# Optimization experiments

Measured on AMD Instinct MI355X. Metric: run time of the kernel, lower is better.

## Reference

```python
import jax, jax.numpy as jnp
from jax import lax
import numpy as np

B, T = 32, 64
E = 64        # embed_dim
U = 32        # num_measurements
D0, D1 = 300, 100
S = 9         # speaker_num
CELL = 64     # output_cell_dim
C = 6         # n_classes
EPS = 1e-12


def setup_inputs() -> dict:
    key = jax.random.key(0)
    ks = jax.random.split(key, 16)
    sc = 1.0 / np.sqrt(E)
    n = lambda i, shape, s=1.0: (jax.random.normal(ks[i], shape, jnp.float32) * s)
    return {
        "x0": n(0, (B, T, D0)),
        "x1": n(1, (B, T, D1)),
        "smask": jax.random.uniform(ks[2], (B, T, S), jnp.float32),
        "umask": jnp.ones((B, T), jnp.float32),
        "W_ih0": n(3, (4 * E, D0), sc), "W_hh0": n(4, (4 * E, E), sc),
        "b_ih0": n(5, (4 * E,), sc), "b_hh0": n(6, (4 * E,), sc),
        "W_ih1": n(7, (4 * E, D1), sc), "W_hh1": n(8, (4 * E, E), sc),
        "b_ih1": n(9, (4 * E,), sc), "b_hh1": n(10, (4 * E,), sc),
        "phase_table": jax.random.uniform(ks[11], (S, E), jnp.float32, -np.pi, np.pi),
        "meas_kernel": jax.random.uniform(ks[12], (U, E, 2), jnp.float32),
        "W1": n(13, (CELL, 2 * U), 0.1), "b1": jnp.zeros((CELL,), jnp.float32),
        "W2": n(14, (C, CELL), 0.1), "b2": jnp.zeros((C,), jnp.float32),
    }


def _lstm_tanh(x, um, Wih, Whh, bih, bhh):
    # torch.nn.LSTMCell (gate order i,f,g,o) + extra tanh applied to h each step;
    # the tanh-ed h is carried as the recurrent state (dropout = identity in eval).
    b, t, _ = x.shape
    e = Whh.shape[1]

    def step(carry, inp):
        h, c = carry
        xt, ut = inp
        g = (xt * ut[:, None]) @ Wih.T + bih + h @ Whh.T + bhh
        i, f, gg, o = jnp.split(g, 4, axis=-1)
        c = jax.nn.sigmoid(f) * c + jax.nn.sigmoid(i) * jnp.tanh(gg)
        h = jnp.tanh(jax.nn.sigmoid(o) * jnp.tanh(c))
        return (h, c), h

    h0 = jnp.zeros((b, e), x.dtype)
    _, hs = lax.scan(step, (h0, h0), (jnp.swapaxes(x, 0, 1), um.T))
    return jnp.swapaxes(hs, 0, 1)  # (B,T,E)


def _measure(amp, phase, kernel):
    # pure state v = cos(phase)*amp + i sin(phase)*amp; rho = |v><v|
    r = jnp.cos(phase) * amp
    im = jnp.sin(phase) * amp
    rho_r = jnp.einsum('bti,btj->btij', r, r) + jnp.einsum('bti,btj->btij', im, im)
    rho_i = jnp.einsum('bti,btj->btij', im, r) - jnp.einsum('bti,btj->btij', r, im)
    u = kernel.shape[0]
    norm = jnp.clip(jnp.linalg.norm(kernel.reshape(u, -1), axis=-1), EPS)
    kn = kernel / norm[:, None, None]
    kr, ki = kn[..., 0], kn[..., 1]
    Pr = jnp.einsum('ui,uj->uij', kr, kr) + jnp.einsum('ui,uj->uij', ki, ki)
    Pi = jnp.einsum('ui,uj->uij', ki, kr) - jnp.einsum('ui,uj->uij', kr, ki)
    return jnp.einsum('btij,uij->btu', rho_r, Pr) - jnp.einsum('btij,uij->btu', rho_i, Pi)


def reference(x0, x1, smask, umask, W_ih0, W_hh0, b_ih0, b_hh0,
              W_ih1, W_hh1, b_ih1, b_hh1, phase_table, meas_kernel,
              W1, b1, W2, b2):
    h0 = _lstm_tanh(x0, umask, W_ih0, W_hh0, b_ih0, b_hh0)
    h1 = _lstm_tanh(x1, umask, W_ih1, W_hh1, b_ih1, b_hh1)
    norm = lambda h: h / jnp.clip(jnp.linalg.norm(h, axis=-1, keepdims=True), EPS)
    phase = phase_table[jnp.argmax(smask, axis=-1)]  # (B,T,E); table shared by both modalities
    m = jnp.concatenate([_measure(norm(h0), phase, meas_kernel),
                         _measure(norm(h1), phase, meas_kernel)], axis=-1)
    hid = jax.nn.relu(m @ W1.T + b1)
    pred = jnp.tanh(hid @ W2.T + b2)
    return jax.nn.log_softmax(pred, axis=2)
```

## Files before the change

### kernel.cpp

```cpp
#include <hip/hip_runtime.h>

typedef unsigned short ushort_t;
typedef unsigned int uint_t;

__device__ __forceinline__ float bf2f(ushort_t v) {
  union { uint_t u; float f; } x; x.u = ((uint_t)v) << 16; return x.f;
}
__device__ __forceinline__ float lo16(uint_t u) {
  union { uint_t u; float f; } x; x.u = u << 16; return x.f;
}
__device__ __forceinline__ float hi16(uint_t u) {
  union { uint_t u; float f; } x; x.u = u & 0xffff0000u; return x.f;
}
__device__ __forceinline__ ushort_t f2bf(float f) {
  union { float f; uint_t u; } x; x.f = f;
  uint_t u = x.u;
  uint_t r = (u + 0x7fffu + ((u >> 16) & 1u)) >> 16;
  return (ushort_t)r;
}
__device__ __forceinline__ bool is_bf16(const void* um) {
  return *(const uint_t*)um == 0x3F803F80u;
}
__device__ __forceinline__ float ld_dual(const void* p, int i, bool isb) {
  return isb ? bf2f(((const ushort_t*)p)[i]) : ((const float*)p)[i];
}
__device__ __forceinline__ float fsig(float x) { return 1.f / (1.f + __expf(-x)); }
__device__ __forceinline__ float ftanh(float x) { return 2.f / (1.f + __expf(-2.f * x)) - 1.f; }

template <int D, bool ISB>
__device__ __forceinline__ void proj_body(
    const void* __restrict__ x, const void* __restrict__ um,
    const void* __restrict__ Wih, const void* __restrict__ bih,
    const void* __restrict__ bhh, float* __restrict__ xw, float* xs)
{
  const int tid = threadIdx.x;
  const int r0 = blockIdx.x * 8;
  for (int i = tid; i < 8 * D; i += 256) {
    const int r = i / D;
    xs[i] = ld_dual(x, r0 * D + i, ISB) * ld_dual(um, r0 + r, ISB);
  }
  __syncthreads();
  float acc[8];
#pragma unroll
  for (int r = 0; r < 8; ++r) acc[r] = 0.f;
#pragma unroll 5
  for (int k = 0; k < D; k += 4) {
    float w0, w1, w2, w3;
    if (ISB) {
      const ushort_t* wr = (const ushort_t*)Wih + tid * D;
      const uint2 wu = *(const uint2*)(wr + k);
      w0 = lo16(wu.x); w1 = hi16(wu.x); w2 = lo16(wu.y); w3 = hi16(wu.y);
    } else {
      const float* wr = (const float*)Wih + tid * D;
      const float4 wv = *(const float4*)(wr + k);
      w0 = wv.x; w1 = wv.y; w2 = wv.z; w3 = wv.w;
    }
#pragma unroll
    for (int r = 0; r < 8; ++r) {
      const float4 xv = *(const float4*)(xs + r * D + k);
      acc[r] = fmaf(xv.x, w0, acc[r]);
      acc[r] = fmaf(xv.y, w1, acc[r]);
      acc[r] = fmaf(xv.z, w2, acc[r]);
      acc[r] = fmaf(xv.w, w3, acc[r]);
    }
  }
  const float bias = ld_dual(bih, tid, ISB) + ld_dual(bhh, tid, ISB);
#pragma unroll
  for (int r = 0; r < 8; ++r)
    xw[(r0 + r) * 256 + tid] = acc[r] + bias;
}

__global__ __launch_bounds__(256) void proj_both(
    const void* __restrict__ x0, const void* __restrict__ x1,
    const void* __restrict__ um,
    const void* __restrict__ Wih0, const void* __restrict__ bih0,
    const void* __restrict__ bhh0,
    const void* __restrict__ Wih1, const void* __restrict__ bih1,
    const void* __restrict__ bhh1,
    float* __restrict__ xw0, float* __restrict__ xw1)
{
  __shared__ __align__(16) float xs[8 * 300];
  const bool isb = is_bf16(um);
  if (blockIdx.y == 0) {
    if (isb) proj_body<300, true>(x0, um, Wih0, bih0, bhh0, xw0, xs);
    else     proj_body<300, false>(x0, um, Wih0, bih0, bhh0, xw0, xs);
  } else {
    if (isb) proj_body<100, true>(x1, um, Wih1, bih1, bhh1, xw1, xs);
    else     proj_body<100, false>(x1, um, Wih1, bih1, bhh1, xw1, xs);
  }
}

__global__ __launch_bounds__(256) void lstm_k(
    const float* __restrict__ xw0, const float* __restrict__ xw1,
    const void* __restrict__ Whh0, const void* __restrict__ Whh1,
    const void* __restrict__ um,
    float* __restrict__ h0r, float* __restrict__ h1r)
{
  const int bid = blockIdx.x;
  const int l = bid >> 5;
  const int b = bid & 31;
  const float* xw = (l ? xw1 : xw0) + b * 64 * 256;
  const void* Whh = (l ? Whh1 : Whh0);
  float* hr = (l ? h1r : h0r) + b * 64 * 64;
  const int tid = threadIdx.x;
  const int e = tid & 63;
  const bool isb = is_bf16(um);

  float w[64];
  if (isb) {
    const ushort_t* wr = (const ushort_t*)Whh + tid * 64;
#pragma unroll
    for (int j = 0; j < 64; j += 8) {
      const uint4 v = *(const uint4*)(wr + j);
      w[j + 0] = lo16(v.x); w[j + 1] = hi16(v.x);
      w[j + 2] = lo16(v.y); w[j + 3] = hi16(v.y);
      w[j + 4] = lo16(v.z); w[j + 5] = hi16(v.z);
      w[j + 6] = lo16(v.w); w[j + 7] = hi16(v.w);
    }
  } else {
    const float* wr = (const float*)Whh + tid * 64;
#pragma unroll
    for (int j = 0; j < 64; j += 4) {
      const float4 v = *(const float4*)(wr + j);
      w[j + 0] = v.x; w[j + 1] = v.y; w[j + 2] = v.z; w[j + 3] = v.w;
    }
  }
  __shared__ __align__(16) float hsh[64];
  __shared__ float gsh[2][256];
  float c = 0.f;
  if (tid < 64) hsh[tid] = 0.f;
  __syncthreads();
  float gin = xw[tid];
  for (int s = 0; s < 64; ++s) {
    float gnext = 0.f;
    if (s < 63) gnext = xw[(s + 1) * 256 + tid];
    float a0 = gin, a1 = 0.f, a2 = 0.f, a3 = 0.f;
#pragma unroll
    for (int j = 0; j < 16; j += 4) {
      const float4 v0 = *(const float4*)(hsh + j);
      const float4 v1 = *(const float4*)(hsh + 16 + j);
      const float4 v2 = *(const float4*)(hsh + 32 + j);
      const float4 v3 = *(const float4*)(hsh + 48 + j);
      a0 = fmaf(w[j + 0], v0.x, a0);  a0 = fmaf(w[j + 1], v0.y, a0);
      a0 = fmaf(w[j + 2], v0.z, a0);  a0 = fmaf(w[j + 3], v0.w, a0);
      a1 = fmaf(w[16 + j + 0], v1.x, a1);  a1 = fmaf(w[16 + j + 1], v1.y, a1);
      a1 = fmaf(w[16 + j + 2], v1.z, a1);  a1 = fmaf(w[16 + j + 3], v1.w, a1);
      a2 = fmaf(w[32 + j + 0], v2.x, a2);  a2 = fmaf(w[32 + j + 1], v2.y, a2);
      a2 = fmaf(w[32 + j + 2], v2.z, a2);  a2 = fmaf(w[32 + j + 3], v2.w, a2);
      a3 = fmaf(w[48 + j + 0], v3.x, a3);  a3 = fmaf(w[48 + j + 1], v3.y, a3);
      a3 = fmaf(w[48 + j + 2], v3.z, a3);  a3 = fmaf(w[48 + j + 3], v3.w, a3);
    }
    const int buf = s & 1;
    gsh[buf][tid] = (a0 + a1) + (a2 + a3);
    __syncthreads();
    const float gi = gsh[buf][e];
    const float gf = gsh[buf][64 + e];
    const float gg = gsh[buf][128 + e];
    const float go = gsh[buf][192 + e];
    c = fsig(gf) * c + fsig(gi) * ftanh(gg);
    const float h = ftanh(fsig(go) * ftanh(c));
    if (tid < 64) hr[s * 64 + e] = h;
    hsh[e] = h;
    gin = gnext;
  }
}

__global__ __launch_bounds__(256) void head_k(
    const float* __restrict__ h0r, const float* __restrict__ h1r,
    const void* __restrict__ smask, const void* __restrict__ um,
    const void* __restrict__ ptab, const void* __restrict__ mker,
    const void* __restrict__ W1, const void* __restrict__ b1,
    const void* __restrict__ W2, const void* __restrict__ b2,
    void* __restrict__ out)
{
  __shared__ float2 knT[64][32];
  __shared__ float w1T[64][64];
  __shared__ float w2T[64][8];
  __shared__ float b1s[64];
  __shared__ float b2s[8];
  __shared__ float rim[4][4][64];
  __shared__ float msh[4][64];
  __shared__ float hidsh[4][64];
  __shared__ float psh[4][8];

  const int tid = threadIdx.x;
  const bool isb = is_bf16(um);
  {
    const int u = tid >> 3, sub = tid & 7;
    float vr[8], vi[8];
    float ssq = 0.f;
#pragma unroll
    for (int q = 0; q < 8; ++q) {
      const int e = sub * 8 + q;
      if (isb) {
        const uint_t kk = ((const uint_t*)mker)[u * 64 + e];
        vr[q] = lo16(kk); vi[q] = hi16(kk);
      } else {
        const float2 kk = ((const float2*)mker)[u * 64 + e];
        vr[q] = kk.x; vi[q] = kk.y;
      }
      ssq = fmaf(vr[q], vr[q], ssq);
      ssq = fmaf(vi[q], vi[q], ssq);
    }
    ssq += __shfl_xor(ssq, 1);
    ssq += __shfl_xor(ssq, 2);
    ssq += __shfl_xor(ssq, 4);
    const float rn = 1.f / fmaxf(sqrtf(ssq), 1e-12f);
#pragma unroll
    for (int q = 0; q < 8; ++q) {
      const int e = sub * 8 + q;
      knT[e][u] = make_float2(vr[q] * rn, vi[q] * rn);
    }
  }
  for (int i = tid; i < 4096; i += 256) {
    const int j = i >> 6, ll = i & 63;
    w1T[ll][j] = ld_dual(W1, i, isb);
  }
  if (tid < 64) b1s[tid] = ld_dual(b1, tid, isb);
  for (int i = tid; i < 384; i += 256) {
    const int cc = i >> 6, j = i & 63;
    w2T[j][cc] = ld_dual(W2, i, isb);
  }
  if (tid < 6) b2s[tid] = ld_dual(b2, tid, isb);
  __syncthreads();

  const int wv = tid >> 6, lane = tid & 63;
  const int item = blockIdx.x * 4 + wv;
  const float h0raw = h0r[item * 64 + lane];
  const float h1raw = h1r[item * 64 + lane];
  float ss0 = h0raw * h0raw, ss1 = h1raw * h1raw;
#pragma unroll
  for (int m = 1; m < 64; m <<= 1) {
    ss0 += __shfl_xor(ss0, m);
    ss1 += __shfl_xor(ss1, m);
  }
  const float h0 = h0raw / fmaxf(sqrtf(ss0), 1e-12f);
  const float h1 = h1raw / fmaxf(sqrtf(ss1), 1e-12f);

  int idx = 0;
  if (lane == 0) {
    float best = -1e30f;
#pragma unroll
    for (int si = 0; si < 9; ++si) {
      const float v = ld_dual(smask, item * 9 + si, isb);
      if (v > best) { best = v; idx = si; }
    }
  }
  idx = __shfl(idx, 0, 64);
  const float ph = ld_dual(ptab, idx * 64 + lane, isb);
  float sr, cr;
  __sincosf(ph, &sr, &cr);
  rim[wv][0][lane] = cr * h0;
  rim[wv][1][lane] = sr * h0;
  rim[wv][2][lane] = cr * h1;
  rim[wv][3][lane] = sr * h1;
  __syncthreads();
  {
    const int u = lane & 31;
    const float* ra = rim[wv][(lane >= 32) ? 2 : 0];
    const float* ia = rim[wv][(lane >= 32) ? 3 : 1];
    float ar = 0.f, ai = 0.f;
#pragma unroll 8
    for (int e = 0; e < 64; ++e) {
      const float2 k = knT[e][u];
      const float rr = ra[e], ii = ia[e];
      ar = fmaf(rr, k.x, ar);
      ar = fmaf(-ii, k.y, ar);
      ai = fmaf(rr, k.y, ai);
      ai = fmaf(ii, k.x, ai);
    }
    msh[wv][lane] = fmaf(ar, ar, ai * ai);
  }
  __syncthreads();
  {
    float acc = b1s[lane];
#pragma unroll 8
    for (int L = 0; L < 64; ++L)
      acc = fmaf(msh[wv][L], w1T[L][lane], acc);
    hidsh[wv][lane] = fmaxf(acc, 0.f);
  }
  __syncthreads();
  if (lane < 6) {
    float a2 = b2s[lane];
#pragma unroll 8
    for (int j = 0; j < 64; ++j)
      a2 = fmaf(hidsh[wv][j], w2T[j][lane], a2);
    psh[wv][lane] = ftanh(a2);
  }
  __syncthreads();
  if (lane < 6) {
    const float p = psh[wv][lane];
    float mx = psh[wv][0];
#pragma unroll
    for (int cc = 1; cc < 6; ++cc) mx = fmaxf(mx, psh[wv][cc]);
    float sum = 0.f;
#pragma unroll
    for (int cc = 0; cc < 6; ++cc) sum += __expf(psh[wv][cc] - mx);
    const float res = p - mx - __logf(sum);
    if (isb) ((ushort_t*)out)[item * 6 + lane] = f2bf(res);
    else     ((float*)out)[item * 6 + lane] = res;
  }
}

extern "C" void kernel_launch(void* const* d_in, const int* in_sizes, int n_in,
                              void* d_out, int out_size, void* d_ws, size_t ws_size,
                              hipStream_t stream)
{
  (void)in_sizes; (void)n_in; (void)out_size; (void)ws_size;
  const void* x0    = d_in[0];
  const void* x1    = d_in[1];
  const void* smask = d_in[2];
  const void* um    = d_in[3];
  const void* Wih0  = d_in[4];
  const void* Whh0  = d_in[5];
  const void* bih0  = d_in[6];
  const void* bhh0  = d_in[7];
  const void* Wih1  = d_in[8];
  const void* Whh1  = d_in[9];
  const void* bih1  = d_in[10];
  const void* bhh1  = d_in[11];
  const void* ptab  = d_in[12];
  const void* mker  = d_in[13];
  const void* W1    = d_in[14];
  const void* b1    = d_in[15];
  const void* W2    = d_in[16];
  const void* b2    = d_in[17];

  float* xw0 = (float*)d_ws;
  float* xw1 = xw0 + 2048 * 256;
  float* h0r = xw1 + 2048 * 256;
  float* h1r = h0r + 2048 * 64;

  hipLaunchKernelGGL(proj_both, dim3(256, 2), dim3(256), 0, stream,
                     x0, x1, um, Wih0, bih0, bhh0, Wih1, bih1, bhh1,
                     xw0, xw1);
  hipLaunchKernelGGL(lstm_k, dim3(64), dim3(256), 0, stream,
                     xw0, xw1, Whh0, Whh1, um, h0r, h1r);
  hipLaunchKernelGGL(head_k, dim3(512), dim3(256), 0, stream,
                     h0r, h1r, smask, um, ptab, mker, W1, b1, W2, b2,
                     d_out);
}
```

Measured before the change: 179.9 us.

## Interleave LSTM gate rows per lane and exchange gates via shuffles

The LSTM recurrence now assigns the four gates of one hidden unit to four adjacent lanes, and the projection kernel writes its gate outputs in that interleaved order. Each lane applies a single sigmoid, computing tanh as 2*sigmoid(2x)-1 for the g gate. The lanes exchange gate values with xor shuffles instead of going through a shared-memory gate buffer. The hidden-state buffer is double-buffered, which leaves one barrier per step instead of the previous store/sync/reload round trip. The cost is extra shuffles and selects per step, plus a harmless out-of-range-free wraparound prefetch of the next input.

```diff
diff --git a/kernel.cpp b/kernel.cpp
--- a/kernel.cpp
+++ b/kernel.cpp
@@ -65,9 +65,10 @@
     }
   }
   const float bias = ld_dual(bih, tid, ISB) + ld_dual(bhh, tid, ISB);
+  const int pos = ((tid & 63) << 2) | (tid >> 6);
 #pragma unroll
   for (int r = 0; r < 8; ++r)
-    xw[(r0 + r) * 256 + tid] = acc[r] + bias;
+    xw[(r0 + r) * 256 + pos] = acc[r] + bias;
 }
 
 __global__ __launch_bounds__(256) void proj_both(
@@ -103,12 +104,16 @@
   const void* Whh = (l ? Whh1 : Whh0);
   float* hr = (l ? h1r : h0r) + b * 64 * 64;
   const int tid = threadIdx.x;
-  const int e = tid & 63;
+  const int wv = tid >> 6, ln = tid & 63;
+  const int t = ln & 3;
+  const int e = wv * 16 + (ln >> 2);
+  const int row = t * 64 + e;
   const bool isb = is_bf16(um);
+  const bool isg = (t == 2);
 
   float w[64];
   if (isb) {
-    const ushort_t* wr = (const ushort_t*)Whh + tid * 64;
+    const ushort_t* wr = (const ushort_t*)Whh + row * 64;
 #pragma unroll
     for (int j = 0; j < 64; j += 8) {
       const uint4 v = *(const uint4*)(wr + j);
@@ -118,29 +123,28 @@
       w[j + 6] = lo16(v.w); w[j + 7] = hi16(v.w);
     }
   } else {
-    const float* wr = (const float*)Whh + tid * 64;
+    const float* wr = (const float*)Whh + row * 64;
 #pragma unroll
     for (int j = 0; j < 64; j += 4) {
       const float4 v = *(const float4*)(wr + j);
       w[j + 0] = v.x; w[j + 1] = v.y; w[j + 2] = v.z; w[j + 3] = v.w;
     }
   }
-  __shared__ __align__(16) float hsh[64];
-  __shared__ float gsh[2][256];
+  __shared__ __align__(16) float hsh[2][64];
   float c = 0.f;
-  if (tid < 64) hsh[tid] = 0.f;
-  __syncthreads();
+  if (tid < 64) hsh[0][tid] = 0.f;
   float gin = xw[tid];
   for (int s = 0; s < 64; ++s) {
-    float gnext = 0.f;
-    if (s < 63) gnext = xw[(s + 1) * 256 + tid];
+    const float gnext = xw[(((s + 1) & 63)) * 256 + tid];
+    __syncthreads();
+    const float* hp = hsh[s & 1];
     float a0 = gin, a1 = 0.f, a2 = 0.f, a3 = 0.f;
 #pragma unroll
     for (int j = 0; j < 16; j += 4) {
-      const float4 v0 = *(const float4*)(hsh + j);
-      const float4 v1 = *(const float4*)(hsh + 16 + j);
-      const float4 v2 = *(const float4*)(hsh + 32 + j);
-      const float4 v3 = *(const float4*)(hsh + 48 + j);
+      const float4 v0 = *(const float4*)(hp + j);
+      const float4 v1 = *(const float4*)(hp + 16 + j);
+      const float4 v2 = *(const float4*)(hp + 32 + j);
+      const float4 v3 = *(const float4*)(hp + 48 + j);
       a0 = fmaf(w[j + 0], v0.x, a0);  a0 = fmaf(w[j + 1], v0.y, a0);
       a0 = fmaf(w[j + 2], v0.z, a0);  a0 = fmaf(w[j + 3], v0.w, a0);
       a1 = fmaf(w[16 + j + 0], v1.x, a1);  a1 = fmaf(w[16 + j + 1], v1.y, a1);
@@ -150,17 +154,26 @@
       a3 = fmaf(w[48 + j + 0], v3.x, a3);  a3 = fmaf(w[48 + j + 1], v3.y, a3);
       a3 = fmaf(w[48 + j + 2], v3.z, a3);  a3 = fmaf(w[48 + j + 3], v3.w, a3);
     }
-    const int buf = s & 1;
-    gsh[buf][tid] = (a0 + a1) + (a2 + a3);
-    __syncthreads();
-    const float gi = gsh[buf][e];
-    const float gf = gsh[buf][64 + e];
-    const float gg = gsh[buf][128 + e];
-    const float go = gsh[buf][192 + e];
-    c = fsig(gf) * c + fsig(gi) * ftanh(gg);
-    const float h = ftanh(fsig(go) * ftanh(c));
-    if (tid < 64) hr[s * 64 + e] = h;
-    hsh[e] = h;
+    const float g = (a0 + a1) + (a2 + a3);
+    const float xv = isg ? (g + g) : g;
+    float y = 1.f / (1.f + __expf(-xv));
+    y = isg ? fmaf(2.f, y, -1.f) : y;
+    const float v1s = __shfl_xor(y, 1);
+    const float v2s = __shfl_xor(y, 2);
+    const float v3s = __shfl_xor(y, 3);
+    const bool s1 = (t & 1), s2 = (t & 2);
+    const float u0 = s1 ? v1s : y;
+    const float u1 = s1 ? y : v1s;
+    const float u2 = s1 ? v3s : v2s;
+    const float u3 = s1 ? v2s : v3s;
+    const float yi = s2 ? u2 : u0;
+    const float yf = s2 ? u3 : u1;
+    const float yg = s2 ? u0 : u2;
+    const float yo = s2 ? u1 : u3;
+    c = fmaf(yf, c, yi * yg);
+    const float h = ftanh(yo * ftanh(c));
+    hsh[(s + 1) & 1][e] = h;
+    if (t == 0) hr[s * 64 + e] = h;
     gin = gnext;
   }
 }
```

New measurement: 175.9 us. 2.2% less time.

## Run LSTM recurrence in a single wavefront with all four gates per thread

Applied to the files above, without the earlier changes.

The LSTM kernel drops from 256 threads to 64, one wavefront, with each thread computing all four gates for its hidden unit. This removes the per-step __syncthreads and the shared-memory gate exchange. The projection output is interleaved so each thread loads its four gate inputs as one float4. The cost is four times the serial FMA work per thread and 256 weight registers per thread, which risks spills. It also relies on wave-synchronous execution for the hsh reads and writes, with no barrier between steps.

```diff
diff --git a/kernel.cpp b/kernel.cpp
--- a/kernel.cpp
+++ b/kernel.cpp
@@ -65,9 +65,10 @@
     }
   }
   const float bias = ld_dual(bih, tid, ISB) + ld_dual(bhh, tid, ISB);
+  const int pos = ((tid & 63) << 2) | (tid >> 6);
 #pragma unroll
   for (int r = 0; r < 8; ++r)
-    xw[(r0 + r) * 256 + tid] = acc[r] + bias;
+    xw[(r0 + r) * 256 + pos] = acc[r] + bias;
 }
 
 __global__ __launch_bounds__(256) void proj_both(
@@ -90,7 +91,7 @@
   }
 }
 
-__global__ __launch_bounds__(256) void lstm_k(
+__global__ __launch_bounds__(64) void lstm_k(
     const float* __restrict__ xw0, const float* __restrict__ xw1,
     const void* __restrict__ Whh0, const void* __restrict__ Whh1,
     const void* __restrict__ um,
@@ -102,66 +103,63 @@
   const float* xw = (l ? xw1 : xw0) + b * 64 * 256;
   const void* Whh = (l ? Whh1 : Whh0);
   float* hr = (l ? h1r : h0r) + b * 64 * 64;
-  const int tid = threadIdx.x;
-  const int e = tid & 63;
+  const int e = threadIdx.x;
   const bool isb = is_bf16(um);
 
-  float w[64];
+  float w[4][64];
   if (isb) {
-    const ushort_t* wr = (const ushort_t*)Whh + tid * 64;
-#pragma unroll
-    for (int j = 0; j < 64; j += 8) {
-      const uint4 v = *(const uint4*)(wr + j);
-      w[j + 0] = lo16(v.x); w[j + 1] = hi16(v.x);
-      w[j + 2] = lo16(v.y); w[j + 3] = hi16(v.y);
-      w[j + 4] = lo16(v.z); w[j + 5] = hi16(v.z);
-      w[j + 6] = lo16(v.w); w[j + 7] = hi16(v.w);
+#pragma unroll
+    for (int t = 0; t < 4; ++t) {
+      const ushort_t* wr = (const ushort_t*)Whh + (t * 64 + e) * 64;
+#pragma unroll
+      for (int j = 0; j < 64; j += 8) {
+        const uint4 v = *(const uint4*)(wr + j);
+        w[t][j + 0] = lo16(v.x); w[t][j + 1] = hi16(v.x);
+        w[t][j + 2] = lo16(v.y); w[t][j + 3] = hi16(v.y);
+        w[t][j + 4] = lo16(v.z); w[t][j + 5] = hi16(v.z);
+        w[t][j + 6] = lo16(v.w); w[t][j + 7] = hi16(v.w);
+      }
     }
   } else {
-    const float* wr = (const float*)Whh + tid * 64;
+#pragma unroll
+    for (int t = 0; t < 4; ++t) {
+      const float* wr = (const float*)Whh + (t * 64 + e) * 64;
+#pragma unroll
+      for (int j = 0; j < 64; j += 4) {
+        const float4 v = *(const float4*)(wr + j);
+        w[t][j + 0] = v.x; w[t][j + 1] = v.y;
+        w[t][j + 2] = v.z; w[t][j + 3] = v.w;
+      }
+    }
+  }
+  __shared__ __align__(16) float hsh[64];
+  hsh[e] = 0.f;
+  float c = 0.f;
+  float4 g4 = *(const float4*)(xw + (e << 2));
+  for (int s = 0; s < 64; ++s) {
+    const float4 g4n = *(const float4*)(xw + (((s + 1) & 63)) * 256 + (e << 2));
+    float ai = g4.x, af = g4.y, ag = g4.z, ao = g4.w;
 #pragma unroll
     for (int j = 0; j < 64; j += 4) {
-      const float4 v = *(const float4*)(wr + j);
-      w[j + 0] = v.x; w[j + 1] = v.y; w[j + 2] = v.z; w[j + 3] = v.w;
-    }
-  }
-  __shared__ __align__(16) float hsh[64];
-  __shared__ float gsh[2][256];
-  float c = 0.f;
-  if (tid < 64) hsh[tid] = 0.f;
-  __syncthreads();
-  float gin = xw[tid];
-  for (int s = 0; s < 64; ++s) {
-    float gnext = 0.f;
-    if (s < 63) gnext = xw[(s + 1) * 256 + tid];
-    float a0 = gin, a1 = 0.f, a2 = 0.f, a3 = 0.f;
-#pragma unroll
-    for (int j = 0; j < 16; j += 4) {
-      const float4 v0 = *(const float4*)(hsh + j);
-      const float4 v1 = *(const float4*)(hsh + 16 + j);
-      const float4 v2 = *(const float4*)(hsh + 32 + j);
-      const float4 v3 = *(const float4*)(hsh + 48 + j);
-      a0 = fmaf(w[j + 0], v0.x, a0);  a0 = fmaf(w[j + 1], v0.y, a0);
-      a0 = fmaf(w[j + 2], v0.z, a0);  a0 = fmaf(w[j + 3], v0.w, a0);
-      a1 = fmaf(w[16 + j + 0], v1.x, a1);  a1 = fmaf(w[16 + j + 1], v1.y, a1);
-      a1 = fmaf(w[16 + j + 2], v1.z, a1);  a1 = fmaf(w[16 + j + 3], v1.w, a1);
-      a2 = fmaf(w[32 + j + 0], v2.x, a2);  a2 = fmaf(w[32 + j + 1], v2.y, a2);
-      a2 = fmaf(w[32 + j + 2], v2.z, a2);  a2 = fmaf(w[32 + j + 3], v2.w, a2);
-      a3 = fmaf(w[48 + j + 0], v3.x, a3);  a3 = fmaf(w[48 + j + 1], v3.y, a3);
-      a3 = fmaf(w[48 + j + 2], v3.z, a3);  a3 = fmaf(w[48 + j + 3], v3.w, a3);
-    }
-    const int buf = s & 1;
-    gsh[buf][tid] = (a0 + a1) + (a2 + a3);
-    __syncthreads();
-    const float gi = gsh[buf][e];
-    const float gf = gsh[buf][64 + e];
-    const float gg = gsh[buf][128 + e];
-    const float go = gsh[buf][192 + e];
-    c = fsig(gf) * c + fsig(gi) * ftanh(gg);
-    const float h = ftanh(fsig(go) * ftanh(c));
-    if (tid < 64) hr[s * 64 + e] = h;
+      const float4 hv = *(const float4*)(hsh + j);
+      ai = fmaf(w[0][j + 0], hv.x, ai); ai = fmaf(w[0][j + 1], hv.y, ai);
+      ai = fmaf(w[0][j + 2], hv.z, ai); ai = fmaf(w[0][j + 3], hv.w, ai);
+      af = fmaf(w[1][j + 0], hv.x, af); af = fmaf(w[1][j + 1], hv.y, af);
+      af = fmaf(w[1][j + 2], hv.z, af); af = fmaf(w[1][j + 3], hv.w, af);
+      ag = fmaf(w[2][j + 0], hv.x, ag); ag = fmaf(w[2][j + 1], hv.y, ag);
+      ag = fmaf(w[2][j + 2], hv.z, ag); ag = fmaf(w[2][j + 3], hv.w, ag);
+      ao = fmaf(w[3][j + 0], hv.x, ao); ao = fmaf(w[3][j + 1], hv.y, ao);
+      ao = fmaf(w[3][j + 2], hv.z, ao); ao = fmaf(w[3][j + 3], hv.w, ao);
+    }
+    const float yi = fsig(ai);
+    const float yf = fsig(af);
+    const float yg = ftanh(ag);
+    const float yo = fsig(ao);
+    c = fmaf(yf, c, yi * yg);
+    const float h = ftanh(yo * ftanh(c));
     hsh[e] = h;
-    gin = gnext;
+    hr[s * 64 + e] = h;
+    g4 = g4n;
   }
 }
 
@@ -334,7 +332,7 @@
   hipLaunchKernelGGL(proj_both, dim3(256, 2), dim3(256), 0, stream,
                      x0, x1, um, Wih0, bih0, bhh0, Wih1, bih1, bhh1,
                      xw0, xw1);
-  hipLaunchKernelGGL(lstm_k, dim3(64), dim3(256), 0, stream,
+  hipLaunchKernelGGL(lstm_k, dim3(64), dim3(64), 0, stream,
                      xw0, xw1, Whh0, Whh1, um, h0r, h1r);
   hipLaunchKernelGGL(head_k, dim3(512), dim3(256), 0, stream,
                      h0r, h1r, smask, um, ptab, mker, W1, b1, W2, b2,
```

New measurement: 214.4 us. +19.2%, slower.
